# Performance work log

Measured on AMD Instinct MI355X. Metric: run time of the kernel, lower is better.

The kernel has to match this reference:

```python
import jax, jax.numpy as jnp
import numpy as np

B, T, IN, H, OUT = 1024, 512, 16, 64, 8


def setup_inputs() -> dict:
    key = jax.random.key(0)
    ks = jax.random.split(key, 7)
    s = 1.0 / np.sqrt(H)
    return {
        "x": jax.random.normal(ks[0], (B, T, IN), dtype=jnp.float32),
        "W_ih": jax.random.normal(ks[1], (4 * H, IN), dtype=jnp.float32) * s,
        "W_hh": jax.random.normal(ks[2], (4 * H, H), dtype=jnp.float32) * s,
        "b_ih": jax.random.normal(ks[3], (4 * H,), dtype=jnp.float32) * s,
        "b_hh": jax.random.normal(ks[4], (4 * H,), dtype=jnp.float32) * s,
        "W_fc": jax.random.normal(ks[5], (OUT, H), dtype=jnp.float32) * s,
        "b_fc": jax.random.normal(ks[6], (OUT,), dtype=jnp.float32) * s,
    }


def reference(x, W_ih, W_hh, b_ih, b_hh, W_fc, b_fc):
    Bq, Tq, _ = x.shape
    Hq = W_hh.shape[1]
    # Precompute input contribution for all timesteps: [T, B, 4H]
    xw = jnp.einsum("bti,gi->tbg", x, W_ih) + b_ih + b_hh

    def step(carry, xw_t):
        h, c = carry
        gates = xw_t + h @ W_hh.T  # [B, 4H]
        i, f, g, o = jnp.split(gates, 4, axis=-1)  # PyTorch gate order i,f,g,o
        i = jax.nn.sigmoid(i)
        f = jax.nn.sigmoid(f)
        g = jnp.tanh(g)
        o = jax.nn.sigmoid(o)
        c = f * c + i * g
        h = o * jnp.tanh(c)
        return (h, c), None

    h0 = jnp.zeros((Bq, Hq), dtype=x.dtype)
    c0 = jnp.zeros((Bq, Hq), dtype=x.dtype)
    (h_last, _), _ = jax.lax.scan(step, (h0, c0), xw)

    # fc on last timestep only, then sigmoid -> [B, 1, OUT]
    out = jax.nn.sigmoid(h_last @ W_fc.T + b_fc)
    return out[:, None, :]
```

## Files before the change

### kernel.cpp

```cpp
#include <hip/hip_runtime.h>
#include <math.h>


#define LSTM_T 512
#define LSTM_IN 16
#define LSTM_H 64
#define LSTM_OUT 8
#define BT 4
#define HSTRIDE 80

#define L2E   1.44269504088896340736f
#define L2E2  2.88539008177792681472f

typedef _Float16 half8  __attribute__((ext_vector_type(8)));
typedef float    floatx4 __attribute__((ext_vector_type(4)));

static __device__ __forceinline__ float fast_rcp(float x) { return __builtin_amdgcn_rcpf(x); }
static __device__ __forceinline__ float fast_exp2(float x) { return __builtin_amdgcn_exp2f(x); }
static __device__ __forceinline__ float sigm2(float p) { return fast_rcp(1.0f + fast_exp2(-p)); }
static __device__ __forceinline__ void pin4(int4& v) {
    asm volatile("" : "+v"(v.x), "+v"(v.y), "+v"(v.z), "+v"(v.w));
}
static __device__ __forceinline__ void pinf4(float4& v) {
    asm volatile("" : "+v"(v.x), "+v"(v.y), "+v"(v.z), "+v"(v.w));
}
static __device__ __forceinline__ void lite_barrier() {
    asm volatile("s_waitcnt lgkmcnt(0)\n\ts_barrier" ::: "memory");
}
static __device__ __forceinline__ unsigned pk2h(float a, float b) {
    return __builtin_bit_cast(unsigned, __builtin_amdgcn_cvt_pkrtz(a, b));
}
static __device__ __forceinline__ half8 to_h8(float4 a, float4 b) {
    uint4 u = make_uint4(pk2h(a.x, a.y), pk2h(a.z, a.w), pk2h(b.x, b.y), pk2h(b.z, b.w));
    return __builtin_bit_cast(half8, u);
}
static __device__ __forceinline__ int4 cvt8h(float4 a, float4 b) {
    return __builtin_bit_cast(int4, to_h8(a, b));
}
static __device__ __forceinline__ float4 ld4(const float* p) {
    return *reinterpret_cast<const float4*>(p);
}
static __device__ __forceinline__ float4 scl4(float4 v, float s) {
    return make_float4(s * v.x, s * v.y, s * v.z, s * v.w);
}
static __device__ __forceinline__ float sel4(floatx4 v, bool r0, bool r1) {
    float lo = r0 ? v[1] : v[0];
    float hi = r0 ? v[3] : v[2];
    return r1 ? hi : lo;
}

__global__ __launch_bounds__(256, 1)
void lstm_mfma_kernel(const float* __restrict__ x,
                      const float* __restrict__ W_ih,
                      const float* __restrict__ W_hh,
                      const float* __restrict__ b_ih,
                      const float* __restrict__ b_hh,
                      const float* __restrict__ W_fc,
                      const float* __restrict__ b_fc,
                      float* __restrict__ out) {
    const int tid   = threadIdx.x;
    const int lane  = tid & 63;
    const int w     = tid >> 6;
    const int q     = lane >> 4;
    const int m     = lane & 15;
    const int b     = m & 3;
    const int r     = m >> 2;
    const bool r0   = (r & 1) != 0;
    const bool r1   = (r & 2) != 0;
    const int jmine = 16 * w + 4 * q + r;
    const int bbase = blockIdx.x * BT;

    __shared__ __align__(128) _Float16 hbuf[2][BT][HSTRIDE];
    __shared__ __align__(16)  float    hfin[BT][LSTM_H];

    int4 Ah[4][2], Ax[4];
    float4 bias4[4];
    #pragma unroll
    for (int tt = 0; tt < 4; ++tt) {
        const float sc = (tt == 2) ? L2E2 : -L2E;
        const int gt = tt * 64 + 16 * w + m;
        #pragma unroll
        for (int c = 0; c < 2; ++c) {
            const float* s = W_hh + gt * LSTM_H + 32 * c + 8 * q;
            Ah[tt][c] = cvt8h(scl4(ld4(s), sc), scl4(ld4(s + 4), sc));
            pin4(Ah[tt][c]);
        }
        float4 xa = make_float4(0.f, 0.f, 0.f, 0.f), xb = xa;
        if (q < 2) {
            const float* s = W_ih + gt * LSTM_IN + 8 * q;
            xa = ld4(s); xb = ld4(s + 4);
        }
        Ax[tt] = cvt8h(scl4(xa, sc), scl4(xb, sc));
        pin4(Ax[tt]);
        const int gb = tt * 64 + 16 * w + 4 * q;
        float4 bi = ld4(b_ih + gb), bh = ld4(b_hh + gb);
        bias4[tt] = make_float4(sc * (bi.x + bh.x), sc * (bi.y + bh.y),
                                sc * (bi.z + bh.z), sc * (bi.w + bh.w));
        pinf4(bias4[tt]);
    }

    if (tid < 128) {
        int bb = tid >> 5, jj = tid & 31;
        reinterpret_cast<int*>(&hbuf[0][bb][0])[jj] = 0;
    }

    const float* xp = x + (size_t)(bbase + b) * LSTM_T * LSTM_IN + 8 * q;
    float4 xA0 = make_float4(0.f, 0.f, 0.f, 0.f), xA1 = xA0;
    float4 xB0 = xA0, xB1 = xA0;
    if (q < 2) {
        xA0 = ld4(xp);              xA1 = ld4(xp + 4);
        xB0 = ld4(xp + LSTM_IN);    xB1 = ld4(xp + LSTM_IN + 4);
    }

    floatx4 accX[4];
    {
        half8 xf = to_h8(xA0, xA1);
        #pragma unroll
        for (int tt = 0; tt < 4; ++tt)
            accX[tt] = __builtin_amdgcn_mfma_f32_16x16x32_f16(
                __builtin_bit_cast(half8, Ax[tt]), xf,
                __builtin_bit_cast(floatx4, bias4[tt]), 0, 0, 0);
    }
    if (q < 2) {
        xA0 = ld4(xp + 2 * LSTM_IN);
        xA1 = ld4(xp + 2 * LSTM_IN + 4);
    }
    __syncthreads();

    float cs = 0.0f, hreg = 0.0f;

#define STEP(T_, X0, X1)                                                        \
    {                                                                           \
        const _Float16* cur = &hbuf[(T_) & 1][0][0];                            \
        _Float16*       nxt = &hbuf[((T_) + 1) & 1][0][0];                      \
               \
        half8 bh0 = *reinterpret_cast<const half8*>(cur + b * HSTRIDE + 8 * q); \
        half8 bh1 = *reinterpret_cast<const half8*>(cur + b * HSTRIDE + 32 + 8 * q); \
        floatx4 acc[4];                                                         \
        _Pragma("unroll")                                                       \
        for (int tt = 0; tt < 4; ++tt)                                          \
            acc[tt] = __builtin_amdgcn_mfma_f32_16x16x32_f16(                   \
                __builtin_bit_cast(half8, Ah[tt][0]), bh0, accX[tt], 0, 0, 0);  \
        _Pragma("unroll")                                                       \
        for (int tt = 0; tt < 4; ++tt)                                          \
            acc[tt] = __builtin_amdgcn_mfma_f32_16x16x32_f16(                   \
                __builtin_bit_cast(half8, Ah[tt][1]), bh1, acc[tt], 0, 0, 0);   \
           \
          \
        if ((T_) + 1 < LSTM_T) {                                                \
            half8 xf = to_h8(X0, X1);                                           \
            _Pragma("unroll")                                                   \
            for (int tt = 0; tt < 4; ++tt)                                      \
                accX[tt] = __builtin_amdgcn_mfma_f32_16x16x32_f16(              \
                    __builtin_bit_cast(half8, Ax[tt]), xf,                      \
                    __builtin_bit_cast(floatx4, bias4[tt]), 0, 0, 0);           \
        }                                                                       \
                                        \
        if (q < 2 && (T_) + 3 < LSTM_T) {                                       \
            X0 = ld4(xp + (size_t)((T_) + 3) * LSTM_IN);                        \
            X1 = ld4(xp + (size_t)((T_) + 3) * LSTM_IN + 4);                    \
        }                                                                       \
                               \
        float ui = sel4(acc[0], r0, r1);                                        \
        float uf = sel4(acc[1], r0, r1);                                        \
        float ug = sel4(acc[2], r0, r1);                                        \
        float uo = sel4(acc[3], r0, r1);                                        \
        float ff = fast_rcp(1.0f + fast_exp2(uf));                              \
        float ii = fast_rcp(1.0f + fast_exp2(ui));                              \
        float gg = fmaf(-2.0f, fast_rcp(1.0f + fast_exp2(ug)), 1.0f);           \
        float oo = fast_rcp(1.0f + fast_exp2(uo));                              \
        cs = fmaf(ff, cs, (L2E2 * ii) * gg);                                    \
        float th = fmaf(-2.0f, fast_rcp(1.0f + fast_exp2(cs)), 1.0f);           \
        hreg = oo * th;                                                         \
                     \
        nxt[b * HSTRIDE + jmine] = (_Float16)hreg;                              \
        lite_barrier();                                                         \
    }

    for (int t = 0; t < LSTM_T; t += 2) {
        STEP(t,     xB0, xB1)
        STEP(t + 1, xA0, xA1)
    }
#undef STEP

    hfin[b][jmine] = hreg;
    __syncthreads();

    if (tid < BT * LSTM_OUT) {
        int bb = tid >> 3, o = tid & 7;
        float s = b_fc[o];
        #pragma unroll
        for (int j4 = 0; j4 < LSTM_H / 4; ++j4) {
            float4 wv = ld4(W_fc + o * LSTM_H + 4 * j4);
            float4 hv = *reinterpret_cast<const float4*>(&hfin[bb][4 * j4]);
            s = fmaf(wv.x, hv.x, s);
            s = fmaf(wv.y, hv.y, s);
            s = fmaf(wv.z, hv.z, s);
            s = fmaf(wv.w, hv.w, s);
        }
        out[(size_t)(bbase + bb) * LSTM_OUT + o] = sigm2(s * L2E);
    }
}

extern "C" void kernel_launch(void* const* d_in, const int* in_sizes, int n_in,
                              void* d_out, int out_size, void* d_ws, size_t ws_size,
                              hipStream_t stream) {
    const float* x    = (const float*)d_in[0];
    const float* W_ih = (const float*)d_in[1];
    const float* W_hh = (const float*)d_in[2];
    const float* b_ih = (const float*)d_in[3];
    const float* b_hh = (const float*)d_in[4];
    const float* W_fc = (const float*)d_in[5];
    const float* b_fc = (const float*)d_in[6];
    float* out = (float*)d_out;

    lstm_mfma_kernel<<<1024 / BT, 256, 0, stream>>>(
        x, W_ih, W_hh, b_ih, b_hh, W_fc, b_fc, out);
}
```

Baseline: 269.4 us.

## Halve batch tile, split gate activations across lane halves via DPP, reorder MFMAs

Reduces the per-block batch tile from 4 to 2 and raises launch bounds to allow two blocks per CU, so more independent recurrences can interleave their latency-bound steps. The freed lanes in the 16x16 MFMA output are used to split the four gate activations: each lane half computes two transcendentals and the partner values are exchanged with a DPP row shift. The f/g MFMAs are issued first so their exponentials can overlap the i/o MFMAs, and s_setprio raises wave priority around the critical section. This doubles the grid size and adds DPP exchanges and selects, and the MFMA work per sample is doubled since half the B columns carry duplicated data.

```diff
diff --git a/kernel.cpp b/kernel.cpp
--- a/kernel.cpp
+++ b/kernel.cpp
@@ -6,7 +6,7 @@
 #define LSTM_IN 16
 #define LSTM_H 64
 #define LSTM_OUT 8
-#define BT 4
+#define BT 2
 #define HSTRIDE 80
 
 #define L2E   1.44269504088896340736f
@@ -48,8 +48,13 @@
     float hi = r0 ? v[3] : v[2];
     return r1 ? hi : lo;
 }
-
-__global__ __launch_bounds__(256, 1)
+static __device__ __forceinline__ float dpp8(float v) {
+    int r = __builtin_amdgcn_update_dpp(0, __builtin_bit_cast(int, v),
+                                        0x128, 0xF, 0xF, false);
+    return __builtin_bit_cast(float, r);
+}
+
+__global__ __launch_bounds__(256, 2)
 void lstm_mfma_kernel(const float* __restrict__ x,
                       const float* __restrict__ W_ih,
                       const float* __restrict__ W_hh,
@@ -63,12 +68,16 @@
     const int w     = tid >> 6;
     const int q     = lane >> 4;
     const int m     = lane & 15;
-    const int b     = m & 3;
-    const int r     = m >> 2;
-    const bool r0   = (r & 1) != 0;
-    const bool r1   = (r & 2) != 0;
-    const int jmine = 16 * w + 4 * q + r;
+    const int b     = m & 1;
+    const int rho   = (m >> 1) & 3;
+    const bool r0   = (rho & 1) != 0;
+    const bool r1   = (rho & 2) != 0;
+    const bool h1   = (m & 8) != 0;
+    const int jmine = 16 * w + 4 * q + rho;
     const int bbase = blockIdx.x * BT;
+
+    const float a1 = h1 ? 1.0f : 0.0f;
+    const float b1 = h1 ? -2.0f : 1.0f;
 
     __shared__ __align__(128) _Float16 hbuf[2][BT][HSTRIDE];
     __shared__ __align__(16)  float    hfin[BT][LSTM_H];
@@ -99,9 +108,8 @@
         pinf4(bias4[tt]);
     }
 
-    if (tid < 128) {
-        int bb = tid >> 5, jj = tid & 31;
-        reinterpret_cast<int*>(&hbuf[0][bb][0])[jj] = 0;
+    if (tid < 80) {
+        reinterpret_cast<int*>(&hbuf[0][0][0])[tid] = 0;
     }
 
     const float* xp = x + (size_t)(bbase + b) * LSTM_T * LSTM_IN + 8 * q;
@@ -136,17 +144,34 @@
                \
         half8 bh0 = *reinterpret_cast<const half8*>(cur + b * HSTRIDE + 8 * q); \
         half8 bh1 = *reinterpret_cast<const half8*>(cur + b * HSTRIDE + 32 + 8 * q); \
-        floatx4 acc[4];                                                         \
-        _Pragma("unroll")                                                       \
-        for (int tt = 0; tt < 4; ++tt)                                          \
-            acc[tt] = __builtin_amdgcn_mfma_f32_16x16x32_f16(                   \
-                __builtin_bit_cast(half8, Ah[tt][0]), bh0, accX[tt], 0, 0, 0);  \
-        _Pragma("unroll")                                                       \
-        for (int tt = 0; tt < 4; ++tt)                                          \
-            acc[tt] = __builtin_amdgcn_mfma_f32_16x16x32_f16(                   \
-                __builtin_bit_cast(half8, Ah[tt][1]), bh1, acc[tt], 0, 0, 0);   \
-           \
-          \
+                \
+        floatx4 accf, accg, acci, acco;                                         \
+        accf = __builtin_amdgcn_mfma_f32_16x16x32_f16(                          \
+            __builtin_bit_cast(half8, Ah[1][0]), bh0, accX[1], 0, 0, 0);        \
+        accg = __builtin_amdgcn_mfma_f32_16x16x32_f16(                          \
+            __builtin_bit_cast(half8, Ah[2][0]), bh0, accX[2], 0, 0, 0);        \
+        accf = __builtin_amdgcn_mfma_f32_16x16x32_f16(                          \
+            __builtin_bit_cast(half8, Ah[1][1]), bh1, accf, 0, 0, 0);           \
+        accg = __builtin_amdgcn_mfma_f32_16x16x32_f16(                          \
+            __builtin_bit_cast(half8, Ah[2][1]), bh1, accg, 0, 0, 0);           \
+        __builtin_amdgcn_s_setprio(1);                                          \
+        float uf = sel4(accf, r0, r1);                                          \
+        float ug = sel4(accg, r0, r1);                                          \
+        float u1 = h1 ? ug : uf;                                                \
+        float e1 = fast_exp2(u1);                                               \
+        acci = __builtin_amdgcn_mfma_f32_16x16x32_f16(                          \
+            __builtin_bit_cast(half8, Ah[0][0]), bh0, accX[0], 0, 0, 0);        \
+        acco = __builtin_amdgcn_mfma_f32_16x16x32_f16(                          \
+            __builtin_bit_cast(half8, Ah[3][0]), bh0, accX[3], 0, 0, 0);        \
+        acci = __builtin_amdgcn_mfma_f32_16x16x32_f16(                          \
+            __builtin_bit_cast(half8, Ah[0][1]), bh1, acci, 0, 0, 0);           \
+        acco = __builtin_amdgcn_mfma_f32_16x16x32_f16(                          \
+            __builtin_bit_cast(half8, Ah[3][1]), bh1, acco, 0, 0, 0);           \
+        float ui = sel4(acci, r0, r1);                                          \
+        float uo = sel4(acco, r0, r1);                                          \
+        float u2 = h1 ? uo : ui;                                                \
+        float e2 = fast_exp2(u2);                                               \
+                 \
         if ((T_) + 1 < LSTM_T) {                                                \
             half8 xf = to_h8(X0, X1);                                           \
             _Pragma("unroll")                                                   \
@@ -160,20 +185,24 @@
             X0 = ld4(xp + (size_t)((T_) + 3) * LSTM_IN);                        \
             X1 = ld4(xp + (size_t)((T_) + 3) * LSTM_IN + 4);                    \
         }                                                                       \
-                               \
-        float ui = sel4(acc[0], r0, r1);                                        \
-        float uf = sel4(acc[1], r0, r1);                                        \
-        float ug = sel4(acc[2], r0, r1);                                        \
-        float uo = sel4(acc[3], r0, r1);                                        \
-        float ff = fast_rcp(1.0f + fast_exp2(uf));                              \
-        float ii = fast_rcp(1.0f + fast_exp2(ui));                              \
-        float gg = fmaf(-2.0f, fast_rcp(1.0f + fast_exp2(ug)), 1.0f);           \
-        float oo = fast_rcp(1.0f + fast_exp2(uo));                              \
-        cs = fmaf(ff, cs, (L2E2 * ii) * gg);                                    \
+        \
+        float act1 = fmaf(b1, fast_rcp(1.0f + e1), a1);                         \
+        float act2 = fast_rcp(1.0f + e2);                                       \
+                                              \
+        float g_in = dpp8(act1);                                                \
+        float o_in = dpp8(act2);                                                \
+                 \
+        float fsel = h1 ? g_in : act1;                            \
+        float isel = h1 ? o_in : act2;                            \
+        float gsel = h1 ? act1 : g_in;                            \
+        float osel = h1 ? act2 : o_in;                            \
+        cs = fmaf(fsel, cs, (L2E2 * isel) * gsel);                              \
         float th = fmaf(-2.0f, fast_rcp(1.0f + fast_exp2(cs)), 1.0f);           \
-        hreg = oo * th;                                                         \
-                     \
+        hreg = osel * th;                                                       \
+           \
+           \
         nxt[b * HSTRIDE + jmine] = (_Float16)hreg;                              \
+        __builtin_amdgcn_s_setprio(0);                                          \
         lite_barrier();                                                         \
     }
 
```

Result: faster. 257.1 us (-4.6%).
